# Optimization experiments

Hardware: AMD Instinct MI355X
Metric: run time of the kernel (lower is better)

The kernel has to match this reference:

```python
import jax, jax.numpy as jnp
import numpy as np


@jax.custom_vjp
def binarize_ste(x):
    return jnp.sign(x)


def _binarize_fwd(x):
    return jnp.sign(x), None


def _binarize_bwd(_, g):
    # straight-through estimator: pass gradient through, clamped to [-1, 1]
    return (jnp.clip(g, -1.0, 1.0),)


binarize_ste.defvjp(_binarize_fwd, _binarize_bwd)


def setup_inputs() -> dict:
    key = jax.random.key(0)
    kx, kw = jax.random.split(key)
    x = jax.random.normal(kx, (32, 128, 64, 64), dtype=jnp.float32)  # NCHW
    weight = jax.random.normal(kw, (256, 128, 3, 3), dtype=jnp.float32)  # OIHW
    return {"x": x, "weight": weight}


def reference(x, weight):
    w_bin = binarize_ste(weight)  # +/-1 (0 where weight==0, matching torch.sign)
    out = jax.lax.conv_general_dilated(
        x, w_bin,
        window_strides=(1, 1),
        padding=((1, 1), (1, 1)),
        dimension_numbers=("NCHW", "OIHW", "NCHW"),
    )
    return out
```

## Files before the change

kernel.cpp:

```cpp
#include <hip/hip_runtime.h>
#include <hip/hip_bf16.h>


typedef short bf16x8 __attribute__((ext_vector_type(8)));
typedef float f32x4 __attribute__((ext_vector_type(4)));

#define XT_ELEMS (32 * 66 * 66 * 128)
#define XT_BYTES (XT_ELEMS * 2)

__device__ __forceinline__ void glds16(const void* g, const void* l) {
    __builtin_amdgcn_global_load_lds(
        (const __attribute__((address_space(1))) void*)g,
        (__attribute__((address_space(3))) void*)l, 16, 0, 0);
}

__global__ void prep_w_kernel(const float* __restrict__ w,
                              __hip_bfloat16* __restrict__ wm) {
    int tid = blockIdx.x * 256 + threadIdx.x;
    int o = tid / 1152;
    int r = tid - o * 1152;
    int j = r >> 7;
    int c = r & 127;
    float v = w[o * 1152 + c * 9 + j];
    float s = (v > 0.f) ? 1.f : ((v < 0.f) ? -1.f : 0.f);
    wm[tid] = __float2bfloat16(s);
}

__global__ void transpose_x_kernel(const float* __restrict__ x,
                                   __hip_bfloat16* __restrict__ xt) {
    __shared__ short tl[64 * 130];
    const int t = threadIdx.x;
    const int n = blockIdx.x >> 6;
    const int h = blockIdx.x & 63;
    const float* xp = x + (size_t)n * 524288 + h * 64;
    for (int i = t; i < 8192; i += 256) {
        int w = i & 63, c = i >> 6;
        tl[w * 130 + c] = (short)__bfloat16_as_ushort(__float2bfloat16(xp[c * 4096 + w]));
    }
    uint* xtn = (uint*)(xt + (size_t)n * 66 * 66 * 128);
    {
        int row = h + 1;
        if (t < 64)       xtn[(row * 66 + 0) * 64 + t] = 0u;
        else if (t < 128) xtn[(row * 66 + 65) * 64 + (t - 64)] = 0u;
    }
    if (h == 0)  for (int i = t; i < 66 * 64; i += 256) xtn[i] = 0u;
    if (h == 63) for (int i = t; i < 66 * 64; i += 256) xtn[65 * 66 * 64 + i] = 0u;
    __syncthreads();
    uint* xo = (uint*)(xt + ((size_t)(n * 66 + h + 1) * 66 + 1) * 128);
    for (int i = t; i < 4096; i += 256) {
        int c2 = i & 63;
        int w = i >> 6;
        xo[w * 64 + c2] = *(const uint*)(tl + w * 130 + c2 * 2);
    }
}

__global__ __launch_bounds__(512, 2) void gemm_kernel(
    const __hip_bfloat16* __restrict__ xt,
    const __hip_bfloat16* __restrict__ wm,
    float* __restrict__ out) {
    __shared__ short As[2][256 * 32];
    __shared__ short Bw[2][264 * 64];

    const int t = threadIdx.x;
    const int lane = t & 63;
    const int wv = t >> 6;
    const int l15 = lane & 15;
    const int quad = lane >> 4;

    const int bid = blockIdx.x;
    const int px_blk = (bid & 7) * 64 + (bid >> 3);
    const int n = px_blk >> 4;
    const int h0 = (px_blk & 15) << 2;

    const int wo = (wv >> 1) * 64;
    const int wpr = (wv & 1) * 2;

    const short* wmS = (const short*)wm;
    const short* xtS = (const short*)xt + (size_t)(n * 66 + h0) * 66 * 128;

    f32x4 acc[4][8] = {};

    auto stageA = [&](int buf, int cc, int j) {
        const short* src = wmS + j * 128 + cc;
#pragma unroll
        for (int i = 0; i < 2; ++i) {
            int g = i * 8 + wv;
            int l = g * 64 + lane;
            int o = l >> 2, q = l & 3;
            glds16(src + o * 1152 + ((q ^ (o & 3)) * 8), &As[buf][g * 512]);
        }
    };
    auto stageB = [&](int buf, int cc, int kh) {
        const short* src = xtS + kh * (66 * 128) + cc;
#pragma unroll
        for (int i = 0; i < 5; ++i) {
            int g = i * 8 + wv;
            if (g < 33) {
                int l = g * 64 + lane;
                int cell = l >> 3, q = l & 7;
                glds16(src + cell * 128 + ((q ^ (cell & 7)) * 8), &Bw[buf][g * 512]);
            }
        }
    };

    stageB(0, 0, 0);
    stageA(0, 0, 0);
    __syncthreads();

    int Ab = 0, Bb = 0;
    for (int s = 0; s < 36; ++s) {
        const int s1 = s + 1;
        if (s1 < 36) {
            const int cc64_1 = (s1 >= 18) ? 64 : 0;
            const int r1 = s1 % 18;
            const int kh1 = r1 / 6;
            const int sub1 = (r1 % 6) / 3;
            const int kw1 = r1 % 3;
            if (s1 % 6 == 0) stageB(Bb ^ 1, cc64_1, kh1);
            stageA(Ab ^ 1, cc64_1 + sub1 * 32, kh1 * 3 + kw1);
        }
        {
            const int r = s % 18;
            const int sub = (r % 6) / 3;
            const int kw = r % 3;
            const short* A_ = As[Ab];
            const short* B_ = Bw[Bb];
            bf16x8 a[4], b[8];
#pragma unroll
            for (int i = 0; i < 4; ++i) {
                int o = wo + i * 16 + l15;
                a[i] = *(const bf16x8*)(A_ + o * 32 + ((quad ^ (o & 3)) * 8));
            }
#pragma unroll
            for (int i = 0; i < 8; ++i) {
                int cell = (wpr + (i >> 2)) * 66 + (i & 3) * 16 + l15 + kw;
                int seg = (sub * 4 + quad) ^ (cell & 7);
                b[i] = *(const bf16x8*)(B_ + cell * 64 + seg * 8);
            }
#pragma unroll
            for (int i = 0; i < 4; ++i)
#pragma unroll
                for (int jj = 0; jj < 8; ++jj)
                    acc[i][jj] = __builtin_amdgcn_mfma_f32_16x16x32_bf16(
                        a[i], b[jj], acc[i][jj], 0, 0, 0);
        }
        __syncthreads();
        Ab ^= 1;
        if (s1 % 6 == 0) Bb ^= 1;
    }

    const int Pbase = px_blk * 256 + (wv & 1) * 128;
#pragma unroll
    for (int i = 0; i < 4; ++i) {
#pragma unroll
        for (int jj = 0; jj < 8; ++jj) {
            const int P = Pbase + jj * 16 + l15;
            const int hw = P & 4095;
            float* op = out + (size_t)n * 1048576 + hw;
#pragma unroll
            for (int r = 0; r < 4; ++r) {
                const int o = wo + i * 16 + quad * 4 + r;
                op[(size_t)o * 4096] = acc[i][jj][r];
            }
        }
    }
}

extern "C" void kernel_launch(void* const* d_in, const int* in_sizes, int n_in,
                              void* d_out, int out_size, void* d_ws, size_t ws_size,
                              hipStream_t stream) {
    const float* x = (const float*)d_in[0];
    const float* w = (const float*)d_in[1];
    float* out = (float*)d_out;
    __hip_bfloat16* xt = (__hip_bfloat16*)d_ws;
    __hip_bfloat16* wm = (__hip_bfloat16*)((char*)d_ws + XT_BYTES);

    prep_w_kernel<<<1152, 256, 0, stream>>>(w, wm);
    transpose_x_kernel<<<2048, 256, 0, stream>>>(x, xt);
    gemm_kernel<<<512, 512, 0, stream>>>(xt, wm, out);
}
```

Baseline: 271.9 us.

## Restructure GEMM pipeline with 64-wide K stages and explicit vmcnt waits

Doubles the weight tile in LDS to 64 channels per stage, so each barrier round runs two MFMA k-substeps and there are half as many stages. The loop is restructured as kh by kw with explicit s_waitcnt vmcnt counts and raw s_barrier, which lets the next stage's loads stay in flight across the barrier instead of being fully drained. It also raises wave priority around the MFMA block. LDS use grows, which may limit the two-blocks-per-CU occupancy, and the hand-counted vmcnt values must match the number of issued loads for results to stay correct.

Result: slower. 396.6 us (+45.8%).

```diff
diff --git a/kernel.cpp b/kernel.cpp
--- a/kernel.cpp
+++ b/kernel.cpp
@@ -7,6 +7,16 @@
 
 #define XT_ELEMS (32 * 66 * 66 * 128)
 #define XT_BYTES (XT_ELEMS * 2)
+
+#define VMW4 asm volatile("s_waitcnt vmcnt(4)" ::: "memory")
+#define VMW9 asm volatile("s_waitcnt vmcnt(9)" ::: "memory")
+#define VMW0 asm volatile("s_waitcnt vmcnt(0)" ::: "memory")
+#define BAR()                                  \
+    do {                                       \
+        asm volatile("" ::: "memory");         \
+        __builtin_amdgcn_s_barrier();          \
+        asm volatile("" ::: "memory");         \
+    } while (0)
 
 __device__ __forceinline__ void glds16(const void* g, const void* l) {
     __builtin_amdgcn_global_load_lds(
@@ -58,7 +68,7 @@
     const __hip_bfloat16* __restrict__ xt,
     const __hip_bfloat16* __restrict__ wm,
     float* __restrict__ out) {
-    __shared__ short As[2][256 * 32];
+    __shared__ short As[2][256 * 64];
     __shared__ short Bw[2][264 * 64];
 
     const int t = threadIdx.x;
@@ -70,83 +80,90 @@
     const int bid = blockIdx.x;
     const int px_blk = (bid & 7) * 64 + (bid >> 3);
     const int n = px_blk >> 4;
-    const int h0 = (px_blk & 15) << 2;
+    const int h0 = (px_blk & 15) * 4;
 
     const int wo = (wv >> 1) * 64;
     const int wpr = (wv & 1) * 2;
 
     const short* wmS = (const short*)wm;
-    const short* xtS = (const short*)xt + (size_t)(n * 66 + h0) * 66 * 128;
+    const short* xtS = (const short*)xt;
 
     f32x4 acc[4][8] = {};
 
-    auto stageA = [&](int buf, int cc, int j) {
-        const short* src = wmS + j * 128 + cc;
+    auto stageA = [&](int pa, int cc, int j) {
 #pragma unroll
-        for (int i = 0; i < 2; ++i) {
+        for (int i = 0; i < 4; ++i) {
             int g = i * 8 + wv;
             int l = g * 64 + lane;
-            int o = l >> 2, q = l & 3;
-            glds16(src + o * 1152 + ((q ^ (o & 3)) * 8), &As[buf][g * 512]);
+            int o = l >> 3, q = l & 7;
+            glds16(wmS + o * 1152 + j * 128 + cc + ((q ^ (o & 7)) * 8),
+                   &As[pa][g * 512]);
         }
     };
-    auto stageB = [&](int buf, int cc, int kh) {
-        const short* src = xtS + kh * (66 * 128) + cc;
+    auto stageB = [&](int pb, int cc, int kh) {
+        const short* src = xtS + ((size_t)(n * 66 + h0 + kh) * 66) * 128 + cc;
 #pragma unroll
         for (int i = 0; i < 5; ++i) {
             int g = i * 8 + wv;
-            if (g < 33) {
-                int l = g * 64 + lane;
-                int cell = l >> 3, q = l & 7;
-                glds16(src + cell * 128 + ((q ^ (cell & 7)) * 8), &Bw[buf][g * 512]);
-            }
+            if (g > 32) g = 32;
+            int l = g * 64 + lane;
+            int cell = l >> 3, q = l & 7;
+            glds16(src + cell * 128 + ((q ^ (cell & 7)) * 8),
+                   &Bw[pb][g * 512]);
         }
     };
 
     stageB(0, 0, 0);
     stageA(0, 0, 0);
-    __syncthreads();
 
-    int Ab = 0, Bb = 0;
-    for (int s = 0; s < 36; ++s) {
-        const int s1 = s + 1;
-        if (s1 < 36) {
-            const int cc64_1 = (s1 >= 18) ? 64 : 0;
-            const int r1 = s1 % 18;
-            const int kh1 = r1 / 6;
-            const int sub1 = (r1 % 6) / 3;
-            const int kw1 = r1 % 3;
-            if (s1 % 6 == 0) stageB(Bb ^ 1, cc64_1, kh1);
-            stageA(Ab ^ 1, cc64_1 + sub1 * 32, kh1 * 3 + kw1);
+    int pa = 0, pb = 0;
+    for (int s = 0; s < 6; ++s) {
+        const int cc = (s >= 3) ? 64 : 0;
+        const int kh = (s >= 3) ? (s - 3) : s;
+        const int sn = s + 1;
+        const int ccn = (sn >= 3) ? 64 : 0;
+        const int khn = (sn >= 3) ? (sn - 3) : sn;
+#pragma unroll
+        for (int kw = 0; kw < 3; ++kw) {
+            if (kw < 2) {
+                stageA(pa ^ 1, cc, kh * 3 + kw + 1);
+                VMW4;
+            } else if (s < 5) {
+                stageA(pa ^ 1, ccn, khn * 3);
+                stageB(pb ^ 1, ccn, khn);
+                VMW9;
+            } else {
+                VMW0;
+            }
+            BAR();
+#pragma unroll
+            for (int kf = 0; kf < 2; ++kf) {
+                bf16x8 a[4], b[8];
+#pragma unroll
+                for (int i = 0; i < 4; ++i) {
+                    int o = wo + i * 16 + l15;
+                    a[i] = *(const bf16x8*)(
+                        &As[pa][o * 64 + (((kf * 4 + quad) ^ (o & 7)) * 8)]);
+                }
+#pragma unroll
+                for (int i = 0; i < 8; ++i) {
+                    int cell = (wpr + (i >> 2)) * 66 + (i & 3) * 16 + l15 + kw;
+                    int seg = (kf * 4 + quad) ^ (cell & 7);
+                    b[i] = *(const bf16x8*)(&Bw[pb][cell * 64 + seg * 8]);
+                }
+                __builtin_amdgcn_s_setprio(1);
+#pragma unroll
+                for (int i = 0; i < 4; ++i)
+#pragma unroll
+                    for (int jj = 0; jj < 8; ++jj)
+                        acc[i][jj] = __builtin_amdgcn_mfma_f32_16x16x32_bf16(
+                            a[i], b[jj], acc[i][jj], 0, 0, 0);
+                __builtin_amdgcn_s_setprio(0);
+            }
+            BAR();
+            pa ^= 1;
         }
-        {
-            const int r = s % 18;
-            const int sub = (r % 6) / 3;
-            const int kw = r % 3;
-            const short* A_ = As[Ab];
-            const short* B_ = Bw[Bb];
-            bf16x8 a[4], b[8];
-#pragma unroll
-            for (int i = 0; i < 4; ++i) {
-                int o = wo + i * 16 + l15;
-                a[i] = *(const bf16x8*)(A_ + o * 32 + ((quad ^ (o & 3)) * 8));
-            }
-#pragma unroll
-            for (int i = 0; i < 8; ++i) {
-                int cell = (wpr + (i >> 2)) * 66 + (i & 3) * 16 + l15 + kw;
-                int seg = (sub * 4 + quad) ^ (cell & 7);
-                b[i] = *(const bf16x8*)(B_ + cell * 64 + seg * 8);
-            }
-#pragma unroll
-            for (int i = 0; i < 4; ++i)
-#pragma unroll
-                for (int jj = 0; jj < 8; ++jj)
-                    acc[i][jj] = __builtin_amdgcn_mfma_f32_16x16x32_bf16(
-                        a[i], b[jj], acc[i][jj], 0, 0, 0);
-        }
-        __syncthreads();
-        Ab ^= 1;
-        if (s1 % 6 == 0) Bb ^= 1;
+        pb ^= 1;
     }
 
     const int Pbase = px_blk * 256 + (wv & 1) * 128;
```
